# Kernel optimization log

Measured on AMD Instinct MI355X. Metric: run time of the kernel, lower is better.

## Reference

```python
import jax, jax.numpy as jnp
import numpy as np

BETA = 0.25

def setup_inputs() -> dict:
    key = jax.random.key(0)
    k1, k2 = jax.random.split(key)
    inputs = jax.random.normal(k1, (64, 32, 32, 64), dtype=jnp.float32)
    w = jax.random.normal(k2, (1024, 64), dtype=jnp.float32)  # codebook [K, D]
    return {"inputs": inputs, "w": w}


def reference(inputs, w):
    D = w.shape[1]
    x = inputs.reshape(-1, D)  # [N, D]
    distances = (
        jnp.sum(x * x, axis=1, keepdims=True)
        - 2.0 * (x @ w.T)
        + jnp.sum(w * w, axis=1)[None, :]
    )
    encodings_indices = jnp.argmax(-distances, axis=1)  # [N], int
    quantized = w[encodings_indices].reshape(inputs.shape)
    e_latent_loss = jnp.mean((jax.lax.stop_gradient(quantized) - inputs) ** 2)
    loss = BETA * e_latent_loss
    # straight-through estimator
    quantized_st = inputs + jax.lax.stop_gradient(quantized - inputs)
    return (quantized_st, loss, encodings_indices, w.T)
```

## Files before the change

### kernel.cpp

```cpp
#include <hip/hip_runtime.h>


#define N_VEC 65536
#define D 64
#define K 1024
#define BETA 0.25f

#define OFF_Q    0
#define OFF_LOSS 4194304
#define OFF_IDX  4194305
#define OFF_WT   4259841

#define WS_WHI  0
#define WS_WLO  131072
#define WS_HNEG 262144

typedef _Float16 v8h __attribute__((ext_vector_type(8)));
typedef float v16f __attribute__((ext_vector_type(16)));
typedef __attribute__((address_space(3))) void lds_void_t;
typedef __attribute__((address_space(1))) const void gbl_void_t;

__global__ __launch_bounds__(256) void vq_prep(const float* __restrict__ w,
                                               char* __restrict__ ws,
                                               float* __restrict__ out_wt) {
  int tid = blockIdx.x * 256 + threadIdx.x;
  {
    int k = tid & 1023, d = tid >> 10;
    out_wt[tid] = w[k * 64 + d];
  }
  {
    int j = tid & 7, l = (tid >> 3) & 63, ks = (tid >> 9) & 3, t = tid >> 11;
    int code = (t << 5) | (l & 31);
    int depth = ks * 16 + ((l >> 5) << 3) + j;
    float v = w[code * 64 + depth];
    _Float16 hi = (_Float16)v;
    _Float16 lo = (_Float16)(v - (float)hi);
    ((_Float16*)(ws + WS_WHI))[tid] = hi;
    ((_Float16*)(ws + WS_WLO))[tid] = lo;
  }
  if (tid < K) {
    const float4* wr = (const float4*)(w + (size_t)tid * D);
    float s = 0.f;
#pragma unroll
    for (int i = 0; i < 16; ++i) {
      float4 v = wr[i];
      s += v.x * v.x + v.y * v.y + v.z * v.z + v.w * v.w;
    }
    ((float*)(ws + WS_HNEG))[tid] = -0.5f * s;
  }
}

#define TPB 256
#define ROWS_PB 128
#define NCH 16

__global__ __launch_bounds__(256) void vq_main(const float* __restrict__ x,
                                               const float* __restrict__ w,
                                               const char* __restrict__ ws,
                                               float* __restrict__ out) {
  __shared__ __align__(16) char lds[37376];
  const int tid = threadIdx.x;
  const int wv = tid >> 6, ln = tid & 63;
  const int col = ln & 31, hi = ln >> 5;
  const int rowBlk = blockIdx.x * ROWS_PB;
  const int myRow = rowBlk + wv * 32 + col;

  v8h ah[4], al[4];
  {
    const float* xr = x + (size_t)myRow * D + hi * 8;
#pragma unroll
    for (int ks = 0; ks < 4; ++ks) {
      float4 v0 = *(const float4*)(xr + ks * 16);
      float4 v1 = *(const float4*)(xr + ks * 16 + 4);
      float xe[8] = {v0.x, v0.y, v0.z, v0.w, v1.x, v1.y, v1.z, v1.w};
#pragma unroll
      for (int j = 0; j < 8; ++j) {
        _Float16 h = (_Float16)xe[j];
        ah[ks][j] = h;
        al[ks][j] = (_Float16)(xe[j] - (float)h);
      }
    }
  }

  auto stage = [&](int c, int p) {
    const char* ghi = ws + WS_WHI + c * 8192;
    const char* glo = ws + WS_WLO + c * 8192;
#pragma unroll
    for (int j = 0; j < 2; ++j) {
      unsigned off = j * 4096 + tid * 16;
      __builtin_amdgcn_global_load_lds((gbl_void_t*)(ghi + off),
                                       (lds_void_t*)(lds + p * 16384 + off), 16, 0, 0);
      __builtin_amdgcn_global_load_lds((gbl_void_t*)(glo + off),
                                       (lds_void_t*)(lds + p * 16384 + 8192 + off), 16, 0, 0);
    }
  };

  v16f best;
  int bidx[16];
#pragma unroll
  for (int r = 0; r < 16; ++r) { best[r] = -3.0e38f; bidx[r] = 0; }

  stage(0, 0);
  __builtin_amdgcn_global_load_lds((gbl_void_t*)(ws + WS_HNEG + tid * 16),
                                   (lds_void_t*)(lds + 32768 + tid * 16), 16, 0, 0);
  asm volatile("s_waitcnt vmcnt(0)" ::: "memory");
  __syncthreads();

  const float* hn_l = (const float*)(lds + 32768);

  for (int c = 0; c < NCH; ++c) {
    const int p = c & 1;
    if (c + 1 < NCH) stage(c + 1, p ^ 1);
    const char* wb = lds + p * 16384;

    const float h0 = hn_l[c * 64 + col];
    const float h1 = hn_l[c * 64 + 32 + col];
    v16f aA, aB;
#pragma unroll
    for (int r = 0; r < 16; ++r) { aA[r] = h0; aB[r] = h1; }

#pragma unroll
    for (int ks = 0; ks < 4; ++ks) {
      v8h bhA = *(const v8h*)(wb + ks * 1024 + ln * 16);
      v8h blA = *(const v8h*)(wb + 8192 + ks * 1024 + ln * 16);
      v8h bhB = *(const v8h*)(wb + 4096 + ks * 1024 + ln * 16);
      v8h blB = *(const v8h*)(wb + 8192 + 4096 + ks * 1024 + ln * 16);
      aA = __builtin_amdgcn_mfma_f32_32x32x16_f16(ah[ks], bhA, aA, 0, 0, 0);
      aB = __builtin_amdgcn_mfma_f32_32x32x16_f16(ah[ks], bhB, aB, 0, 0, 0);
      aA = __builtin_amdgcn_mfma_f32_32x32x16_f16(al[ks], bhA, aA, 0, 0, 0);
      aB = __builtin_amdgcn_mfma_f32_32x32x16_f16(al[ks], bhB, aB, 0, 0, 0);
      aA = __builtin_amdgcn_mfma_f32_32x32x16_f16(ah[ks], blA, aA, 0, 0, 0);
      aB = __builtin_amdgcn_mfma_f32_32x32x16_f16(ah[ks], blB, aB, 0, 0, 0);
    }

    const int kgA = c * 64 + col;
    const int kgB = c * 64 + 32 + col;
#pragma unroll
    for (int r = 0; r < 16; ++r) {
      if (aA[r] > best[r]) { best[r] = aA[r]; bidx[r] = kgA; }
      if (aB[r] > best[r]) { best[r] = aB[r]; bidx[r] = kgB; }
    }

    asm volatile("s_waitcnt vmcnt(0)" ::: "memory");
    __syncthreads();
  }

#pragma unroll
  for (int m = 1; m <= 16; m <<= 1) {
#pragma unroll
    for (int r = 0; r < 16; ++r) {
      float ov = __shfl_xor(best[r], m, 64);
      int oi = __shfl_xor(bidx[r], m, 64);
      if (ov > best[r] || (ov == best[r] && oi < bidx[r])) { best[r] = ov; bidx[r] = oi; }
    }
  }

  int* res = (int*)(lds + 36864);
  if (col == 0) {
#pragma unroll
    for (int r = 0; r < 16; ++r) {
      int row = (r & 3) + 8 * (r >> 2) + 4 * hi;
      res[wv * 32 + row] = bidx[r];
    }
  }
  {
    const int row = wv * 32 + col;
    const unsigned swz = (unsigned)((row & 7) << 4);
#pragma unroll
    for (int ks = 0; ks < 4; ++ks) {
      float4 q0 = make_float4((float)ah[ks][0] + (float)al[ks][0],
                              (float)ah[ks][1] + (float)al[ks][1],
                              (float)ah[ks][2] + (float)al[ks][2],
                              (float)ah[ks][3] + (float)al[ks][3]);
      float4 q1 = make_float4((float)ah[ks][4] + (float)al[ks][4],
                              (float)ah[ks][5] + (float)al[ks][5],
                              (float)ah[ks][6] + (float)al[ks][6],
                              (float)ah[ks][7] + (float)al[ks][7]);
      unsigned b = (unsigned)(row * 256 + (ks * 16 + hi * 8) * 4);
      *(float4*)((char*)lds + (b ^ swz)) = q0;
      *(float4*)((char*)lds + ((b + 16) ^ swz)) = q1;
    }
  }
  __syncthreads();

  const int erow = ln >> 1;
  const int half = ln & 1;
  const int growLocal = wv * 32 + erow;
  const int grow = rowBlk + growLocal;
  const int bi = res[growLocal];
  if (half == 0) out[OFF_IDX + grow] = (float)bi;

  const float4* qsrc = (const float4*)(w + (size_t)bi * D + half * 32);
  float4* qdst = (float4*)(out + OFF_Q + (size_t)grow * D + half * 32);
  const unsigned eswz = (unsigned)((growLocal & 7) << 4);
  float sse = 0.f;
#pragma unroll
  for (int i = 0; i < 8; ++i) {
    float4 q = qsrc[i];
    qdst[i] = q;
    unsigned b = (unsigned)(growLocal * 256 + half * 128 + i * 16);
    float4 xv4 = *(const float4*)((const char*)lds + (b ^ eswz));
    float d0 = q.x - xv4.x, d1 = q.y - xv4.y;
    float d2 = q.z - xv4.z, d3 = q.w - xv4.w;
    sse += d0 * d0 + d1 * d1 + d2 * d2 + d3 * d3;
  }
#pragma unroll
  for (int off = 32; off >= 1; off >>= 1) sse += __shfl_xor(sse, off, 64);
  if (ln == 0) atomicAdd(out + OFF_LOSS, sse * (BETA / (float)(N_VEC * D)));
}

extern "C" void kernel_launch(void* const* d_in, const int* in_sizes, int n_in,
                              void* d_out, int out_size, void* d_ws, size_t ws_size,
                              hipStream_t stream) {
  const float* x = (const float*)d_in[0];
  const float* w = (const float*)d_in[1];
  float* out = (float*)d_out;
  char* ws = (char*)d_ws;

  hipMemsetAsync(out + OFF_LOSS, 0, sizeof(float), stream);
  vq_prep<<<256, 256, 0, stream>>>(w, ws, out + OFF_WT);
  vq_main<<<N_VEC / ROWS_PB, TPB, 0, stream>>>(x, w, ws, out);
}
```

Baseline: 130.2 us.

## Split codebook across two waves per row tile and restructure prep kernel

The main kernel now uses 512 threads, with each pair of waves handling half of the codebook for the same 32 rows, and the partial argmax results are merged through LDS. The aim is more parallelism and latency hiding per block, at the cost of larger LDS use and possibly lower block occupancy. The prep kernel is rewritten to stage rows of w in LDS, giving coalesced reads for the transpose and the fp16 split, and it zeroes the loss itself instead of using a separate memset.

```diff
diff --git a/kernel.cpp b/kernel.cpp
--- a/kernel.cpp
+++ b/kernel.cpp
@@ -22,48 +22,71 @@
 
 __global__ __launch_bounds__(256) void vq_prep(const float* __restrict__ w,
                                                char* __restrict__ ws,
-                                               float* __restrict__ out_wt) {
-  int tid = blockIdx.x * 256 + threadIdx.x;
+                                               float* __restrict__ out) {
+  __shared__ float s[2048];
+  const int t = blockIdx.x, tid = threadIdx.x;
+
+  const float4* src = (const float4*)(w + (size_t)t * 2048);
+  float4 a = src[tid];
+  float4 b = src[tid + 256];
+  ((float4*)s)[tid] = a;
+  ((float4*)s)[tid + 256] = b;
+
+  float p0 = a.x * a.x + a.y * a.y + a.z * a.z + a.w * a.w;
+  float p1 = b.x * b.x + b.y * b.y + b.z * b.z + b.w * b.w;
+#pragma unroll
+  for (int m = 1; m <= 8; m <<= 1) {
+    p0 += __shfl_xor(p0, m, 64);
+    p1 += __shfl_xor(p1, m, 64);
+  }
+  float* hn = (float*)(ws + WS_HNEG);
+  if ((tid & 15) == 0) {
+    hn[t * 32 + (tid >> 4)] = -0.5f * p0;
+    hn[t * 32 + 16 + (tid >> 4)] = -0.5f * p1;
+  }
+  if (t == 0 && tid == 0) out[OFF_LOSS] = 0.f;
+  __syncthreads();
+
   {
-    int k = tid & 1023, d = tid >> 10;
-    out_wt[tid] = w[k * 64 + d];
-  }
+    const int ks = tid >> 6, l = tid & 63;
+    const float* r0 = s + (l & 31) * 64 + ks * 16 + ((l >> 5) << 3);
+    v8h hv, lv;
+#pragma unroll
+    for (int j = 0; j < 8; ++j) {
+      float v = r0[j];
+      _Float16 h = (_Float16)v;
+      hv[j] = h;
+      lv[j] = (_Float16)(v - (float)h);
+    }
+    const size_t eoff = ((size_t)(t * 4 + ks) * 64 + l) * 16;
+    *(v8h*)(ws + WS_WHI + eoff) = hv;
+    *(v8h*)(ws + WS_WLO + eoff) = lv;
+  }
+
   {
-    int j = tid & 7, l = (tid >> 3) & 63, ks = (tid >> 9) & 3, t = tid >> 11;
-    int code = (t << 5) | (l & 31);
-    int depth = ks * 16 + ((l >> 5) << 3) + j;
-    float v = w[code * 64 + depth];
-    _Float16 hi = (_Float16)v;
-    _Float16 lo = (_Float16)(v - (float)hi);
-    ((_Float16*)(ws + WS_WHI))[tid] = hi;
-    ((_Float16*)(ws + WS_WLO))[tid] = lo;
-  }
-  if (tid < K) {
-    const float4* wr = (const float4*)(w + (size_t)tid * D);
-    float s = 0.f;
-#pragma unroll
-    for (int i = 0; i < 16; ++i) {
-      float4 v = wr[i];
-      s += v.x * v.x + v.y * v.y + v.z * v.z + v.w * v.w;
-    }
-    ((float*)(ws + WS_HNEG))[tid] = -0.5f * s;
+    const int d = tid >> 2, k0 = (tid & 3) * 8;
+#pragma unroll
+    for (int j = 0; j < 8; ++j)
+      out[OFF_WT + d * 1024 + t * 32 + k0 + j] = s[(k0 + j) * 64 + d];
   }
 }
 
-#define TPB 256
+#define TPB 512
 #define ROWS_PB 128
-#define NCH 16
-
-__global__ __launch_bounds__(256) void vq_main(const float* __restrict__ x,
-                                               const float* __restrict__ w,
-                                               const char* __restrict__ ws,
-                                               float* __restrict__ out) {
-  __shared__ __align__(16) char lds[37376];
+#define NPH 8
+
+__global__ __launch_bounds__(TPB, 4) void vq_main(const float* __restrict__ x,
+                                                  const float* __restrict__ w,
+                                                  const char* __restrict__ ws,
+                                                  float* __restrict__ out) {
+  __shared__ __align__(16) char lds[71680];
   const int tid = threadIdx.x;
   const int wv = tid >> 6, ln = tid & 63;
+  const int rt = wv >> 1;
+  const int h = wv & 1;
   const int col = ln & 31, hi = ln >> 5;
   const int rowBlk = blockIdx.x * ROWS_PB;
-  const int myRow = rowBlk + wv * 32 + col;
+  const int myRow = rowBlk + rt * 32 + col;
 
   v8h ah[4], al[4];
   {
@@ -75,23 +98,23 @@
       float xe[8] = {v0.x, v0.y, v0.z, v0.w, v1.x, v1.y, v1.z, v1.w};
 #pragma unroll
       for (int j = 0; j < 8; ++j) {
-        _Float16 h = (_Float16)xe[j];
-        ah[ks][j] = h;
-        al[ks][j] = (_Float16)(xe[j] - (float)h);
+        _Float16 hh = (_Float16)xe[j];
+        ah[ks][j] = hh;
+        al[ks][j] = (_Float16)(xe[j] - (float)hh);
       }
     }
   }
 
-  auto stage = [&](int c, int p) {
-    const char* ghi = ws + WS_WHI + c * 8192;
-    const char* glo = ws + WS_WLO + c * 8192;
-#pragma unroll
-    for (int j = 0; j < 2; ++j) {
-      unsigned off = j * 4096 + tid * 16;
-      __builtin_amdgcn_global_load_lds((gbl_void_t*)(ghi + off),
-                                       (lds_void_t*)(lds + p * 16384 + off), 16, 0, 0);
-      __builtin_amdgcn_global_load_lds((gbl_void_t*)(glo + off),
-                                       (lds_void_t*)(lds + p * 16384 + 8192 + off), 16, 0, 0);
+  auto stage = [&](int p, int buf) {
+#pragma unroll
+    for (int hh = 0; hh < 2; ++hh) {
+      const int c = hh * 8 + p;
+      const unsigned off = (unsigned)tid * 16;
+      char* dst = lds + buf * 32768 + hh * 16384;
+      __builtin_amdgcn_global_load_lds((gbl_void_t*)(ws + WS_WHI + c * 8192 + off),
+                                       (lds_void_t*)(dst + off), 16, 0, 0);
+      __builtin_amdgcn_global_load_lds((gbl_void_t*)(ws + WS_WLO + c * 8192 + off),
+                                       (lds_void_t*)(dst + 8192 + off), 16, 0, 0);
     }
   };
 
@@ -101,17 +124,19 @@
   for (int r = 0; r < 16; ++r) { best[r] = -3.0e38f; bidx[r] = 0; }
 
   stage(0, 0);
-  __builtin_amdgcn_global_load_lds((gbl_void_t*)(ws + WS_HNEG + tid * 16),
-                                   (lds_void_t*)(lds + 32768 + tid * 16), 16, 0, 0);
+  if (tid < 256)
+    __builtin_amdgcn_global_load_lds((gbl_void_t*)(ws + WS_HNEG + tid * 16),
+                                     (lds_void_t*)(lds + 65536 + tid * 16), 16, 0, 0);
   asm volatile("s_waitcnt vmcnt(0)" ::: "memory");
   __syncthreads();
 
-  const float* hn_l = (const float*)(lds + 32768);
-
-  for (int c = 0; c < NCH; ++c) {
-    const int p = c & 1;
-    if (c + 1 < NCH) stage(c + 1, p ^ 1);
-    const char* wb = lds + p * 16384;
+  const float* hn_l = (const float*)(lds + 65536);
+
+  for (int p = 0; p < NPH; ++p) {
+    const int buf = p & 1;
+    if (p + 1 < NPH) stage(p + 1, buf ^ 1);
+    const char* wb = lds + buf * 32768 + h * 16384;
+    const int c = h * 8 + p;
 
     const float h0 = hn_l[c * 64 + col];
     const float h1 = hn_l[c * 64 + 32 + col];
@@ -155,16 +180,19 @@
     }
   }
 
-  int* res = (int*)(lds + 36864);
+  float* resS = (float*)(lds + 69632);
+  int*   resI = (int*)(lds + 70656);
   if (col == 0) {
 #pragma unroll
     for (int r = 0; r < 16; ++r) {
       int row = (r & 3) + 8 * (r >> 2) + 4 * hi;
-      res[wv * 32 + row] = bidx[r];
-    }
-  }
-  {
-    const int row = wv * 32 + col;
+      int row128 = rt * 32 + row;
+      resS[row128 * 2 + h] = best[r];
+      resI[row128 * 2 + h] = bidx[r];
+    }
+  }
+  if (h == 0) {
+    const int row = rt * 32 + col;
     const unsigned swz = (unsigned)((row & 7) << 4);
 #pragma unroll
     for (int ks = 0; ks < 4; ++ks) {
@@ -183,23 +211,22 @@
   }
   __syncthreads();
 
-  const int erow = ln >> 1;
-  const int half = ln & 1;
-  const int growLocal = wv * 32 + erow;
-  const int grow = rowBlk + growLocal;
-  const int bi = res[growLocal];
-  if (half == 0) out[OFF_IDX + grow] = (float)bi;
-
-  const float4* qsrc = (const float4*)(w + (size_t)bi * D + half * 32);
-  float4* qdst = (float4*)(out + OFF_Q + (size_t)grow * D + half * 32);
-  const unsigned eswz = (unsigned)((growLocal & 7) << 4);
+  const int row128 = tid >> 2, part = tid & 3;
+  const int grow = rowBlk + row128;
+  const float s0 = resS[row128 * 2], s1v = resS[row128 * 2 + 1];
+  const int bi = (s1v > s0) ? resI[row128 * 2 + 1] : resI[row128 * 2];
+  if (part == 0) out[OFF_IDX + grow] = (float)bi;
+
+  const float4* qsrc = (const float4*)(w + (size_t)bi * D + part * 16);
+  float4* qdst = (float4*)(out + OFF_Q + (size_t)grow * D + part * 16);
+  const unsigned eswz = (unsigned)((row128 & 7) << 4);
   float sse = 0.f;
 #pragma unroll
-  for (int i = 0; i < 8; ++i) {
+  for (int i = 0; i < 4; ++i) {
     float4 q = qsrc[i];
     qdst[i] = q;
-    unsigned b = (unsigned)(growLocal * 256 + half * 128 + i * 16);
-    float4 xv4 = *(const float4*)((const char*)lds + (b ^ eswz));
+    unsigned bb = (unsigned)(row128 * 256 + part * 64 + i * 16);
+    float4 xv4 = *(const float4*)((const char*)lds + (bb ^ eswz));
     float d0 = q.x - xv4.x, d1 = q.y - xv4.y;
     float d2 = q.z - xv4.z, d3 = q.w - xv4.w;
     sse += d0 * d0 + d1 * d1 + d2 * d2 + d3 * d3;
@@ -217,7 +244,6 @@
   float* out = (float*)d_out;
   char* ws = (char*)d_ws;
 
-  hipMemsetAsync(out + OFF_LOSS, 0, sizeof(float), stream);
-  vq_prep<<<256, 256, 0, stream>>>(w, ws, out + OFF_WT);
+  vq_prep<<<32, 256, 0, stream>>>(w, ws, out);
   vq_main<<<N_VEC / ROWS_PB, TPB, 0, stream>>>(x, w, ws, out);
 }
```

New measurement: 155.0 us. 1.19x slower.
